# Kernel tuning notes

Measured on AMD Instinct MI355X. Metric: run time of the kernel, lower is better.

The kernel has to match this reference:

```python
import jax, jax.numpy as jnp
import numpy as np

N_NODES = 30000
N_EDGES = 480000
C = 32          # channel multiplicity of hidden irreps (32x0e + 32x1o)
L = 3           # graph_net_steps
H = 64          # radial MLP hidden width
NB = 8          # num radial basis functions
NS = 5          # num_species
R_MAX = 4.0
AVG_NEIGH = 16.0
N_PATHS = 5     # tensor-product paths per layer


def setup_inputs() -> dict:
    key = jax.random.key(0)
    ks = jax.random.split(key, 16)

    def w(k, shape, fan_in):
        return jax.random.normal(k, shape, jnp.float32) / np.sqrt(fan_in)

    return {
        "vectors": jax.random.normal(ks[0], (N_EDGES, 3), jnp.float32),
        "node_specie": jax.random.randint(ks[1], (N_NODES,), 0, NS),
        "senders": jax.random.randint(ks[2], (N_EDGES,), 0, N_NODES),
        "receivers": jax.random.randint(ks[3], (N_EDGES,), 0, N_NODES),
        "emb": jax.random.normal(ks[4], (NS, C), jnp.float32),
        "w_rad1": w(ks[5], (L, NB, H), NB),
        "w_rad2": w(ks[6], (L, H, H), H),
        "w_rad_out": w(ks[7], (L, H, N_PATHS * C), H),
        "w_lin_s": w(ks[8], (L, 2 * C, 2 * C), 2 * C),
        "w_lin_v": w(ks[9], (L, 3 * C, C), 3 * C),
        "w_sc_s": w(ks[10], (L, NS, C, 2 * C), C),
        "w_sc_v": w(ks[11], (L, NS, C, C), C),
        "w_out1": w(ks[12], (C, 16), C),
        "w_out2": w(ks[13], (16, 1), 16),
    }


def _envelope(x, p=6):
    # smooth polynomial cutoff, = 1 at x=0, = 0 (with zero derivs) at x=1
    u = (1.0 - (p + 1) * (p + 2) / 2 * x**p + p * (p + 2) * x**(p + 1)
         - p * (p + 1) / 2 * x**(p + 2))
    return jnp.where(x < 1.0, u, 0.0)


def _radial_basis(lengths):
    # bessel radial basis [E, NB] with smooth cutoff envelope
    n = jnp.arange(1, NB + 1, dtype=jnp.float32)
    x = lengths / R_MAX
    b = np.sqrt(2.0 / R_MAX) * jnp.sin(n * np.pi * x[:, None]) \
        / jnp.maximum(lengths, 1e-9)[:, None]
    return b * _envelope(x)[:, None]


def reference(vectors, node_specie, senders, receivers, emb, w_rad1, w_rad2,
              w_rad_out, w_lin_s, w_lin_v, w_sc_s, w_sc_v, w_out1, w_out2):
    vectors = vectors / R_MAX                       # as in original __call__
    lengths = jnp.linalg.norm(vectors, axis=-1)
    nhat = vectors / jnp.maximum(lengths, 1e-9)[:, None]   # unit edge vectors
    rb = _radial_basis(lengths)                     # [E, NB]

    s = emb[node_specie]                            # [N, C] scalars (0e)
    v = jnp.zeros((s.shape[0], C, 3), s.dtype)      # [N, C, 3] vectors (1o)

    for l in range(L):
        # radial MLP -> per-path, per-channel edge weights
        h = jax.nn.silu(rb @ w_rad1[l])
        h = jax.nn.silu(h @ w_rad2[l])
        wgt = (h @ w_rad_out[l]).reshape(-1, N_PATHS, C)        # [E, 5, C]

        s_u = s[senders]                                         # [E, C]
        v_u = v[senders]                                         # [E, C, 3]
        ndv = jnp.einsum('ed,ecd->ec', nhat, v_u)                # <n, v>

        # CG tensor-product message paths with spherical harmonics of n
        p0 = wgt[:, 0] * s_u                                     # 0e x Y0 -> 0e
        p1 = wgt[:, 1] * ndv                                     # 1o x Y1 -> 0e
        p2 = wgt[:, 2][:, :, None] * (s_u[:, :, None] * nhat[:, None, :])  # 0e x Y1 -> 1o
        p3 = wgt[:, 3][:, :, None] * v_u                         # 1o x Y0 -> 1o
        p4 = wgt[:, 4][:, :, None] * (nhat[:, None, :] * ndv[:, :, None] - v_u / 3.0)  # 1o x Y2 -> 1o

        agg_s = jax.ops.segment_sum(jnp.concatenate([p0, p1], 1), receivers,
                                    num_segments=N_NODES) / AVG_NEIGH      # [N, 2C]
        agg_v = jax.ops.segment_sum(jnp.concatenate([p2, p3, p4], 1), receivers,
                                    num_segments=N_NODES) / AVG_NEIGH      # [N, 3C, 3]

        sg = agg_s @ w_lin_s[l]                                  # [N, 2C]: C feats + C gates
        vn = jnp.einsum('npd,pc->ncd', agg_v, w_lin_v[l])        # [N, C, 3]
        # self-connection: per-species linear (== tp with species one-hot)
        sg = sg + jnp.einsum('nc,nck->nk', s, w_sc_s[l][node_specie])
        vn = vn + jnp.einsum('ncd,nck->nkd', v, w_sc_v[l][node_specie])

        s_new, gates = jnp.split(sg, 2, axis=1)
        s = jax.nn.silu(s_new)                                   # even activation
        v = jax.nn.silu(gates)[:, :, None] * vn                  # gated 1o

    e = (s @ w_out1) @ w_out2            # Linear '16x0e' -> Linear '0e'
    return e[:, 0]                        # per-node energy [N]
```

## Files before the change

### kernel.cpp

```cpp
#include <hip/hip_runtime.h>
#include <math.h>

#define NNODES 30000
#define NEDGES 480000
#define NC 32
#define NL 3
#define NH 64
#define NBASIS 8
#define NSPEC 5
#define INV_AVG 0.0625f

typedef _Float16 half2v __attribute__((ext_vector_type(2)));
typedef _Float16 half4v __attribute__((ext_vector_type(4)));
typedef _Float16 half8v __attribute__((ext_vector_type(8)));
typedef float    float4v __attribute__((ext_vector_type(4)));
typedef unsigned int uint32;

__device__ __forceinline__ float silu_f(float x) {
    return x / (1.f + __expf(-x));
}
__device__ __forceinline__ float rdlane(float v, int k) {
    return __uint_as_float(__builtin_amdgcn_readlane(__float_as_uint(v), k));
}
__device__ __forceinline__ half2v u2h(uint32 u) {
    union { uint32 u; half2v h; } x; x.u = u; return x.h;
}


__global__ void count_kernel(const int* __restrict__ receivers, int* __restrict__ deg) {
    int e = blockIdx.x * blockDim.x + threadIdx.x;
    if (e >= NEDGES) return;
    atomicAdd(&deg[receivers[e]], 1);
}

__global__ void scan_kernel(const int* __restrict__ deg, int* __restrict__ rowstart) {
    __shared__ int lsum[256];
    __shared__ int loff[256];
    int t = threadIdx.x;
    int lo = t * 118;
    int hi = min(lo + 118, NNODES);
    int s = 0;
    for (int i = lo; i < hi; ++i) s += deg[i];
    lsum[t] = s;
    __syncthreads();
    if (t == 0) {
        int run = 0;
        for (int i = 0; i < 256; ++i) { loff[i] = run; run += lsum[i]; }
    }
    __syncthreads();
    int run = loff[t];
    for (int i = lo; i < hi; ++i) { rowstart[i] = run; run += deg[i]; }
    if (t == 0) rowstart[NNODES] = NEDGES;
}

__global__ void copy_cursor_kernel(const int* __restrict__ rowstart, int* __restrict__ cursor) {
    int i = blockIdx.x * blockDim.x + threadIdx.x;
    if (i < NNODES) cursor[i] = rowstart[i];
}

__global__ void fill_kernel(const int* __restrict__ receivers,
                            int* __restrict__ cursor, int* __restrict__ epos) {
    int e = blockIdx.x * blockDim.x + threadIdx.x;
    if (e >= NEDGES) return;
    epos[e] = atomicAdd(&cursor[receivers[e]], 1);
}

__global__ void geom_perm_kernel(const float* __restrict__ vec,
                                 const int* __restrict__ senders,
                                 const int* __restrict__ epos,
                                 float* __restrict__ nh_perm,
                                 int* __restrict__ snd_perm,
                                 float* __restrict__ rb_perm) {
    int e = blockIdx.x * blockDim.x + threadIdx.x;
    if (e >= NEDGES) return;
    float vx = vec[3*e+0] * 0.25f;
    float vy = vec[3*e+1] * 0.25f;
    float vz = vec[3*e+2] * 0.25f;
    float len = sqrtf(vx*vx + vy*vy + vz*vz);
    float inv = 1.f / fmaxf(len, 1e-9f);
    int p = epos[e];
    *(float4*)(nh_perm + (size_t)p*4) = make_float4(vx*inv, vy*inv, vz*inv, 0.f);
    snd_perm[p] = senders[e];
    float x = len * 0.25f;
    float x3 = x*x*x;
    float x6 = x3*x3;
    float x7 = x6*x;
    float x8 = x7*x;
    float env = (x < 1.f) ? (1.f - 28.f*x6 + 48.f*x7 - 21.f*x8) : 0.f;
    float scale = 0.7071067811865476f * inv * env;
    float rbv[8];
    #pragma unroll
    for (int i = 0; i < NBASIS; ++i)
        rbv[i] = scale * sinf((float)(i+1) * 3.14159265358979f * x);
    *(float4*)(rb_perm + (size_t)p*8)     = make_float4(rbv[0], rbv[1], rbv[2], rbv[3]);
    *(float4*)(rb_perm + (size_t)p*8 + 4) = make_float4(rbv[4], rbv[5], rbv[6], rbv[7]);
}

__global__ void prepw_kernel(const float* __restrict__ w1, const float* __restrict__ w2,
                             const float* __restrict__ w3,
                             float* __restrict__ w1t, _Float16* __restrict__ w2f,
                             _Float16* __restrict__ w3f) {
    int t = blockIdx.x * blockDim.x + threadIdx.x;
    if (t < NL * 64 * 8) {
        int l = t / 512, r = t % 512, k = r >> 3, b = r & 7;
        w1t[t] = w1[l * 512 + b * 64 + k];
    }
    int u = t - NL * 64 * 8;
    if (u >= 0 && u < NL * 2 * 4 * 64 * 8) {
        int e = u & 7, lane = (u >> 3) & 63, nt = (u >> 9) & 3, ks = (u >> 11) & 1, l = u >> 12;
        int k = ks * 32 + ((lane >> 4) << 3) + e;
        int col = nt * 16 + (lane & 15);
        w2f[u] = (_Float16)w2[l * 4096 + k * 64 + col];
    }
    int v = t - NL * 64 * 8 - NL * 2 * 4 * 64 * 8;
    if (v >= 0 && v < NL * 2 * 10 * 64 * 8) {
        int q = v / 5120, rem = v % 5120;
        int l = q >> 1, ks = q & 1;
        int nt = rem >> 9, lane = (rem >> 3) & 63, e = rem & 7;
        int k = ks * 32 + ((lane >> 4) << 3) + e;
        int col = nt * 16 + (lane & 15);
        w3f[v] = (_Float16)w3[l * 10240 + k * 160 + col];
    }
}

__global__ void init_kernel(const int* __restrict__ specie,
                            const float* __restrict__ emb,
                            _Float16* __restrict__ s) {
    int t = blockIdx.x * blockDim.x + threadIdx.x;
    if (t >= NNODES * NC) return;
    int n = t >> 5;
    int c = t & 31;
    s[t] = (_Float16)emb[specie[n] * NC + c];
}

__global__ __launch_bounds__(256) void mlpm_kernel(
    const float* __restrict__ rb_perm,
    const float* __restrict__ w1t,
    const _Float16* __restrict__ w2f,
    const _Float16* __restrict__ w3f,
    _Float16* __restrict__ wgt16)
{
    __shared__ float w1lds[512];
    __shared__ __align__(16) _Float16 lds2[4][2688];

    for (int t = threadIdx.x; t < 512; t += 256) w1lds[t] = w1t[t];
    __syncthreads();

    int lane = threadIdx.x & 63;
    int wid  = threadIdx.x >> 6;
    int c16 = lane & 15;
    int kg  = lane >> 4;
    int ibase = blockIdx.x * 64 + wid * 16;
    int g = blockIdx.x * 4 + wid;

    float4 ra4 = *(const float4*)(rb_perm + (size_t)(ibase + c16) * 8);
    float4 rb4 = *(const float4*)(rb_perm + (size_t)(ibase + c16) * 8 + 4);

    half8v a0, a1;
    #pragma unroll
    for (int e = 0; e < 8; ++e) {
        const float* wr0 = w1lds + (kg * 8 + e) * 8;
        float d0;
        d0 = ra4.x * wr0[0];
        d0 = fmaf(ra4.y, wr0[1], d0);
        d0 = fmaf(ra4.z, wr0[2], d0);
        d0 = fmaf(ra4.w, wr0[3], d0);
        d0 = fmaf(rb4.x, wr0[4], d0);
        d0 = fmaf(rb4.y, wr0[5], d0);
        d0 = fmaf(rb4.z, wr0[6], d0);
        d0 = fmaf(rb4.w, wr0[7], d0);
        a0[e] = (_Float16)silu_f(d0);
        const float* wr1 = w1lds + (32 + kg * 8 + e) * 8;
        float d1;
        d1 = ra4.x * wr1[0];
        d1 = fmaf(ra4.y, wr1[1], d1);
        d1 = fmaf(ra4.z, wr1[2], d1);
        d1 = fmaf(ra4.w, wr1[3], d1);
        d1 = fmaf(rb4.x, wr1[4], d1);
        d1 = fmaf(rb4.y, wr1[5], d1);
        d1 = fmaf(rb4.z, wr1[6], d1);
        d1 = fmaf(rb4.w, wr1[7], d1);
        a1[e] = (_Float16)silu_f(d1);
    }

    _Float16* tw = &lds2[wid][0];
    float4v zero4 = {0.f, 0.f, 0.f, 0.f};
    #pragma unroll
    for (int nt = 0; nt < 4; ++nt) {
        half8v b0 = *(const half8v*)(w2f + (size_t)(nt) * 512 + lane * 8);
        half8v b1 = *(const half8v*)(w2f + (size_t)(4 + nt) * 512 + lane * 8);
        float4v acc = __builtin_amdgcn_mfma_f32_16x16x32_f16(a0, b0, zero4, 0, 0, 0);
        acc = __builtin_amdgcn_mfma_f32_16x16x32_f16(a1, b1, acc, 0, 0, 0);
        #pragma unroll
        for (int r = 0; r < 4; ++r)
            tw[(kg * 4 + r) * 72 + nt * 16 + c16] = (_Float16)silu_f(acc[r]);
    }

    half8v a2 = *(const half8v*)(tw + c16 * 72 + kg * 8);
    half8v a3 = *(const half8v*)(tw + c16 * 72 + 32 + kg * 8);

    #pragma unroll
    for (int nt = 0; nt < 10; ++nt) {
        half8v b0 = *(const half8v*)(w3f + (size_t)(nt) * 512 + lane * 8);
        half8v b1 = *(const half8v*)(w3f + (size_t)(10 + nt) * 512 + lane * 8);
        float4v acc = __builtin_amdgcn_mfma_f32_16x16x32_f16(a2, b0, zero4, 0, 0, 0);
        acc = __builtin_amdgcn_mfma_f32_16x16x32_f16(a3, b1, acc, 0, 0, 0);
        int slot;
        if (nt < 4)      slot = nt * 32 + 2 * c16;
        else if (nt < 8) slot = (nt - 4) * 32 + 2 * c16 + 1;
        else             slot = 128 + (nt - 8) * 16 + c16;
        #pragma unroll
        for (int r = 0; r < 4; ++r)
            tw[(kg * 4 + r) * 168 + slot] = (_Float16)acc[r];
    }

    _Float16* gout = wgt16 + (size_t)g * 2560;
    #pragma unroll
    for (int u = 0; u < 5; ++u) {
        int g4 = u * 64 + lane;
        int edge = g4 / 20;
        int part = g4 % 20;
        half8v vv = *(const half8v*)(tw + edge * 168 + part * 8);
        *(half8v*)(gout + edge * 160 + part * 8) = vv;
    }
}

__global__ __launch_bounds__(512) void gather_tp_kernel(
    const _Float16* __restrict__ wgt16,
    const float* __restrict__ nh_perm,
    const int* __restrict__ snd_perm,
    const int* __restrict__ rowstart, const int* __restrict__ deg,
    const _Float16* __restrict__ s_in, const _Float16* __restrict__ v_in,
    float* __restrict__ agg_s,
    float* __restrict__ agg_v)
{
    int lane = threadIdx.x & 63;
    int wid  = threadIdx.x >> 6;
    int n = blockIdx.x * 8 + wid;
    if (n >= NNODES) return;

    int c = lane & 31;
    int half = lane >> 5;

    float accS = 0.f;
    float aVa0 = 0.f, aVa1 = 0.f, aVa2 = 0.f;
    float aVb0 = 0.f, aVb1 = 0.f, aVb2 = 0.f;

    int start = rowstart[n];
    int cnt   = deg[n];

    float4 nh_c = make_float4(0.f, 0.f, 0.f, 0.f);
    float d0_c = 0.f, d1_c = 0.f, d2_c = 0.f;
    float su_c = 0.f, v0_c = 0.f, v1_c = 0.f, v2_c = 0.f;
    if (cnt > 0) {
        int snd0 = snd_perm[start];
        nh_c = *(const float4*)(nh_perm + (size_t)start * 4);
        size_t gb = (size_t)(start >> 4) * 2560 + (size_t)(start & 15) * 160;
        half2v pr = u2h(*(const uint32*)(wgt16 + gb + lane * 2));
        d0_c = (float)pr.x;
        d1_c = (float)pr.y;
        d2_c = (float)wgt16[gb + 128 + c];
        su_c = (float)s_in[(size_t)snd0 * NC + c];
        v0_c = (float)v_in[(size_t)snd0 * 96 + c];
        v1_c = (float)v_in[(size_t)snd0 * 96 + 32 + c];
        v2_c = (float)v_in[(size_t)snd0 * 96 + 64 + c];
    }

    for (int i = 0; i < cnt; ++i) {
        float4 nh = nh_c;
        float d0 = d0_c, d1 = d1_c, d2f = d2_c;
        float su = su_c, v0 = v0_c, v1 = v1_c, v2 = v2_c;

        if (i + 1 < cnt) {
            int idx1 = start + i + 1;
            int snd1 = snd_perm[idx1];
            nh_c = *(const float4*)(nh_perm + (size_t)idx1 * 4);
            size_t gb1 = (size_t)(idx1 >> 4) * 2560 + (size_t)(idx1 & 15) * 160;
            half2v pr1 = u2h(*(const uint32*)(wgt16 + gb1 + lane * 2));
            d0_c = (float)pr1.x;
            d1_c = (float)pr1.y;
            d2_c = (float)wgt16[gb1 + 128 + c];
            su_c = (float)s_in[(size_t)snd1 * NC + c];
            v0_c = (float)v_in[(size_t)snd1 * 96 + c];
            v1_c = (float)v_in[(size_t)snd1 * 96 + 32 + c];
            v2_c = (float)v_in[(size_t)snd1 * 96 + 64 + c];
        }

        float ndv = nh.x * v0;
        ndv = fmaf(nh.y, v1, ndv);
        ndv = fmaf(nh.z, v2, ndv);

        float sSel = half ? ndv : su;
        accS = fmaf(d0, sSel, accS);
        float scale = half ? d1 : d1 * su;
        float f0 = half ? v0 : nh.x;
        float f1 = half ? v1 : nh.y;
        float f2 = half ? v2 : nh.z;
        aVa0 = fmaf(scale, f0, aVa0);
        aVa1 = fmaf(scale, f1, aVa1);
        aVa2 = fmaf(scale, f2, aVa2);
        float m4 = half ? 0.f : d2f;
        aVb0 = fmaf(m4, fmaf(nh.x, ndv, -v0 * (1.f / 3.f)), aVb0);
        aVb1 = fmaf(m4, fmaf(nh.y, ndv, -v1 * (1.f / 3.f)), aVb1);
        aVb2 = fmaf(m4, fmaf(nh.z, ndv, -v2 * (1.f / 3.f)), aVb2);
    }

    agg_s[(size_t)n * 64 + lane] = accS;
    float* av = agg_v + (size_t)n * 288;
    if (half == 0) {
        av[c * 3 + 0] = aVa0; av[c * 3 + 1] = aVa1; av[c * 3 + 2] = aVa2;
        av[(64 + c) * 3 + 0] = aVb0; av[(64 + c) * 3 + 1] = aVb1; av[(64 + c) * 3 + 2] = aVb2;
    } else {
        av[(32 + c) * 3 + 0] = aVa0; av[(32 + c) * 3 + 1] = aVa1; av[(32 + c) * 3 + 2] = aVa2;
    }
}

__global__ __launch_bounds__(256) void node_kernel(
    const int* __restrict__ specie,
    const float* __restrict__ agg_s, const float* __restrict__ agg_v,
    const _Float16* __restrict__ s_in,  const _Float16* __restrict__ v_in,
    const float* __restrict__ wls,
    const float* __restrict__ wlv,
    const float* __restrict__ wscs,
    const float* __restrict__ wscv,
    _Float16* __restrict__ s_out, _Float16* __restrict__ v_out)
{
    __shared__ float sAV[4][288];
    __shared__ float sVO[4][96];

    int lane = threadIdx.x & 63;
    int wid  = threadIdx.x >> 6;
    int n = blockIdx.x * 4 + wid;
    if (n >= NNODES) return;
    int sp = specie[n];

    const float* av = agg_v + (size_t)n * 288;
    sAV[wid][lane]       = av[lane];
    sAV[wid][64 + lane]  = av[64 + lane];
    sAV[wid][128 + lane] = av[128 + lane];
    sAV[wid][192 + lane] = av[192 + lane];
    if (lane < 32) sAV[wid][256 + lane] = av[256 + lane];
    const _Float16* vo = v_in + (size_t)n * 96;
    if (lane < 32) {
        sVO[wid][lane]      = (float)vo[lane];
        sVO[wid][32 + lane] = (float)vo[32 + lane];
        sVO[wid][64 + lane] = (float)vo[64 + lane];
    }

    float asv = agg_s[(size_t)n * 64 + lane];
    float sv  = (float)s_in[(size_t)n * 32 + (lane & 31)];

    __syncthreads();

    float sg = 0.f;
    #pragma unroll
    for (int j = 0; j < 64; ++j)
        sg = fmaf(rdlane(asv, j), wls[j * 64 + lane], sg);
    sg *= INV_AVG;
    const float* ws = wscs + (size_t)sp * 32 * 64;
    #pragma unroll
    for (int j = 0; j < 32; ++j)
        sg = fmaf(rdlane(sv, j), ws[j * 64 + lane], sg);
    float act  = silu_f(sg);
    float gate = __shfl(act, (lane & 31) + 32);

    int c = lane & 31;
    int h = lane >> 5;
    float vn1 = 0.f, vn2 = 0.f;
    #pragma unroll
    for (int p = 0; p < 96; ++p) {
        float w = wlv[p * 32 + c];
        vn1 = fmaf(sAV[wid][3 * p + h], w, vn1);
        vn2 = fmaf(sAV[wid][3 * p + 2], w, vn2);
    }
    vn1 *= INV_AVG; vn2 *= INV_AVG;
    const float* wv = wscv + (size_t)sp * 32 * 32;
    #pragma unroll
    for (int j = 0; j < 32; ++j) {
        float w = wv[j * 32 + c];
        vn1 = fmaf(sVO[wid][h * 32 + j], w, vn1);
        vn2 = fmaf(sVO[wid][64 + j],     w, vn2);
    }

    if (lane < 32) s_out[(size_t)n * 32 + lane] = (_Float16)act;
    v_out[(size_t)n * 96 + h * 32 + c] = (_Float16)(gate * vn1);
    if (h == 0) v_out[(size_t)n * 96 + 64 + c] = (_Float16)(gate * vn2);
}

__global__ void out_kernel(const _Float16* __restrict__ s,
                           const float* __restrict__ w1,
                           const float* __restrict__ w2,
                           float* __restrict__ out) {
    int n = blockIdx.x * blockDim.x + threadIdx.x;
    if (n >= NNODES) return;
    float sv[NC];
    #pragma unroll
    for (int c = 0; c < NC; ++c) sv[c] = (float)s[(size_t)n * NC + c];
    float e = 0.f;
    #pragma unroll
    for (int j = 0; j < 16; ++j) {
        float tj = 0.f;
        #pragma unroll
        for (int c = 0; c < NC; ++c) tj += sv[c] * w1[c * 16 + j];
        e += tj * w2[j];
    }
    out[n] = e;
}

extern "C" void kernel_launch(void* const* d_in, const int* in_sizes, int n_in,
                              void* d_out, int out_size, void* d_ws, size_t ws_size,
                              hipStream_t stream) {
    const float* vectors   = (const float*)d_in[0];
    const int*   specie    = (const int*)  d_in[1];
    const int*   senders   = (const int*)  d_in[2];
    const int*   receivers = (const int*)  d_in[3];
    const float* emb       = (const float*)d_in[4];
    const float* w_rad1    = (const float*)d_in[5];
    const float* w_rad2    = (const float*)d_in[6];
    const float* w_rad_out = (const float*)d_in[7];
    const float* w_lin_s   = (const float*)d_in[8];
    const float* w_lin_v   = (const float*)d_in[9];
    const float* w_sc_s    = (const float*)d_in[10];
    const float* w_sc_v    = (const float*)d_in[11];
    const float* w_out1    = (const float*)d_in[12];
    const float* w_out2    = (const float*)d_in[13];

    char* base = (char*)d_ws;
    size_t off = 0;
    auto alloc = [&](size_t bytes) { char* q = base + off; off += (bytes + 255) & ~(size_t)255; return q; };

    float*    nh_perm  = (float*)alloc((size_t)NEDGES * 4 * 4);
    float*    rb_perm  = (float*)alloc((size_t)NEDGES * 8 * 4);
    int*      snd_perm = (int*)alloc((size_t)NEDGES * 4);
    int*      epos     = (int*)alloc((size_t)NEDGES * 4);
    _Float16* s_a      = (_Float16*)alloc((size_t)NNODES * NC * 2);
    _Float16* v_a      = (_Float16*)alloc((size_t)NNODES * NC * 3 * 2);
    _Float16* s_b      = (_Float16*)alloc((size_t)NNODES * NC * 2);
    _Float16* v_b      = (_Float16*)alloc((size_t)NNODES * NC * 3 * 2);
    float*    aggs     = (float*)alloc((size_t)NNODES * 2 * NC * 4);
    float*    aggv     = (float*)alloc((size_t)NNODES * 3 * NC * 3 * 4);
    int* deg        = (int*)alloc((size_t)NNODES * 4);
    int* rowstart   = (int*)alloc((size_t)(NNODES + 4) * 4);
    int* cursor     = (int*)alloc((size_t)NNODES * 4);
    float*    w1t      = (float*)alloc((size_t)NL * 64 * 8 * 4);
    _Float16* w2f      = (_Float16*)alloc((size_t)NL * 2 * 4 * 64 * 8 * 2);
    _Float16* w3f      = (_Float16*)alloc((size_t)NL * 2 * 10 * 64 * 8 * 2);
    _Float16* wgt16    = (_Float16*)alloc((size_t)NEDGES * 160 * 2);
    if (off > ws_size) return;

    (void)hipMemsetAsync(deg, 0, NNODES * sizeof(int), stream);
    count_kernel<<<(NEDGES + 255) / 256, 256, 0, stream>>>(receivers, deg);
    scan_kernel<<<1, 256, 0, stream>>>(deg, rowstart);
    copy_cursor_kernel<<<(NNODES + 255) / 256, 256, 0, stream>>>(rowstart, cursor);
    fill_kernel<<<(NEDGES + 255) / 256, 256, 0, stream>>>(receivers, cursor, epos);
    geom_perm_kernel<<<(NEDGES + 255) / 256, 256, 0, stream>>>(
        vectors, senders, epos, nh_perm, snd_perm, rb_perm);
    int prep_n = NL * 64 * 8 + NL * 2 * 4 * 64 * 8 + NL * 2 * 10 * 64 * 8;
    prepw_kernel<<<(prep_n + 255) / 256, 256, 0, stream>>>(
        w_rad1, w_rad2, w_rad_out, w1t, w2f, w3f);

    init_kernel<<<(NNODES * NC + 255) / 256, 256, 0, stream>>>(specie, emb, s_a);
    (void)hipMemsetAsync(v_a, 0, (size_t)NNODES * NC * 3 * 2, stream);

    _Float16* si = s_a; _Float16* vi = v_a; _Float16* so = s_b; _Float16* vo = v_b;
    for (int l = 0; l < NL; ++l) {
        mlpm_kernel<<<NEDGES / 64, 256, 0, stream>>>(
            rb_perm,
            w1t + (size_t)l * 512,
            w2f + (size_t)l * 4096,
            w3f + (size_t)l * 10240,
            wgt16);
        gather_tp_kernel<<<(NNODES + 7) / 8, 512, 0, stream>>>(
            wgt16, nh_perm, snd_perm, rowstart, deg, si, vi, aggs, aggv);
        node_kernel<<<(NNODES + 3) / 4, 256, 0, stream>>>(
            specie, aggs, aggv, si, vi,
            w_lin_s + (size_t)l * 64 * 64,
            w_lin_v + (size_t)l * 96 * 32,
            w_sc_s + (size_t)l * NSPEC * NC * 64,
            w_sc_v + (size_t)l * NSPEC * NC * NC,
            so, vo);
        _Float16* ts = si; si = so; so = ts;
        _Float16* tv = vi; vi = vo; vo = tv;
    }

    out_kernel<<<(NNODES + 255) / 256, 256, 0, stream>>>(si, w_out1, w_out2, (float*)d_out);
}
```

Baseline: 720.4 us.

## Merge CSR count and fill passes; store aggregates in fp16

The separate count and fill atomic passes, plus the cursor copy kernel, are replaced by a single atomic pass whose return value gives each edge's local slot. The global position is then rebuilt from the row start during the geometry permute. This removes two kernel launches and one pass of atomics over the edges. Separately, the per-node aggregate buffers written by the gather kernel and read by the node kernel are switched from fp32 to fp16, halving that traffic at some cost in accumulated precision.

```diff
diff --git a/kernel.cpp b/kernel.cpp
--- a/kernel.cpp
+++ b/kernel.cpp
@@ -27,10 +27,11 @@
 }
 
 
-__global__ void count_kernel(const int* __restrict__ receivers, int* __restrict__ deg) {
+__global__ void fill_kernel(const int* __restrict__ receivers,
+                            int* __restrict__ deg, int* __restrict__ epos) {
     int e = blockIdx.x * blockDim.x + threadIdx.x;
     if (e >= NEDGES) return;
-    atomicAdd(&deg[receivers[e]], 1);
+    epos[e] = atomicAdd(&deg[receivers[e]], 1);
 }
 
 __global__ void scan_kernel(const int* __restrict__ deg, int* __restrict__ rowstart) {
@@ -53,20 +54,10 @@
     if (t == 0) rowstart[NNODES] = NEDGES;
 }
 
-__global__ void copy_cursor_kernel(const int* __restrict__ rowstart, int* __restrict__ cursor) {
-    int i = blockIdx.x * blockDim.x + threadIdx.x;
-    if (i < NNODES) cursor[i] = rowstart[i];
-}
-
-__global__ void fill_kernel(const int* __restrict__ receivers,
-                            int* __restrict__ cursor, int* __restrict__ epos) {
-    int e = blockIdx.x * blockDim.x + threadIdx.x;
-    if (e >= NEDGES) return;
-    epos[e] = atomicAdd(&cursor[receivers[e]], 1);
-}
-
 __global__ void geom_perm_kernel(const float* __restrict__ vec,
                                  const int* __restrict__ senders,
+                                 const int* __restrict__ receivers,
+                                 const int* __restrict__ rowstart,
                                  const int* __restrict__ epos,
                                  float* __restrict__ nh_perm,
                                  int* __restrict__ snd_perm,
@@ -78,7 +69,7 @@
     float vz = vec[3*e+2] * 0.25f;
     float len = sqrtf(vx*vx + vy*vy + vz*vz);
     float inv = 1.f / fmaxf(len, 1e-9f);
-    int p = epos[e];
+    int p = rowstart[receivers[e]] + epos[e];
     *(float4*)(nh_perm + (size_t)p*4) = make_float4(vx*inv, vy*inv, vz*inv, 0.f);
     snd_perm[p] = senders[e];
     float x = len * 0.25f;
@@ -231,8 +222,8 @@
     const int* __restrict__ snd_perm,
     const int* __restrict__ rowstart, const int* __restrict__ deg,
     const _Float16* __restrict__ s_in, const _Float16* __restrict__ v_in,
-    float* __restrict__ agg_s,
-    float* __restrict__ agg_v)
+    _Float16* __restrict__ agg_s,
+    _Float16* __restrict__ agg_v)
 {
     int lane = threadIdx.x & 63;
     int wid  = threadIdx.x >> 6;
@@ -305,19 +296,19 @@
         aVb2 = fmaf(m4, fmaf(nh.z, ndv, -v2 * (1.f / 3.f)), aVb2);
     }
 
-    agg_s[(size_t)n * 64 + lane] = accS;
-    float* av = agg_v + (size_t)n * 288;
+    agg_s[(size_t)n * 64 + lane] = (_Float16)accS;
+    _Float16* av = agg_v + (size_t)n * 288;
     if (half == 0) {
-        av[c * 3 + 0] = aVa0; av[c * 3 + 1] = aVa1; av[c * 3 + 2] = aVa2;
-        av[(64 + c) * 3 + 0] = aVb0; av[(64 + c) * 3 + 1] = aVb1; av[(64 + c) * 3 + 2] = aVb2;
+        av[c * 3 + 0] = (_Float16)aVa0; av[c * 3 + 1] = (_Float16)aVa1; av[c * 3 + 2] = (_Float16)aVa2;
+        av[(64 + c) * 3 + 0] = (_Float16)aVb0; av[(64 + c) * 3 + 1] = (_Float16)aVb1; av[(64 + c) * 3 + 2] = (_Float16)aVb2;
     } else {
-        av[(32 + c) * 3 + 0] = aVa0; av[(32 + c) * 3 + 1] = aVa1; av[(32 + c) * 3 + 2] = aVa2;
+        av[(32 + c) * 3 + 0] = (_Float16)aVa0; av[(32 + c) * 3 + 1] = (_Float16)aVa1; av[(32 + c) * 3 + 2] = (_Float16)aVa2;
     }
 }
 
 __global__ __launch_bounds__(256) void node_kernel(
     const int* __restrict__ specie,
-    const float* __restrict__ agg_s, const float* __restrict__ agg_v,
+    const _Float16* __restrict__ agg_s, const _Float16* __restrict__ agg_v,
     const _Float16* __restrict__ s_in,  const _Float16* __restrict__ v_in,
     const float* __restrict__ wls,
     const float* __restrict__ wlv,
@@ -334,12 +325,12 @@
     if (n >= NNODES) return;
     int sp = specie[n];
 
-    const float* av = agg_v + (size_t)n * 288;
-    sAV[wid][lane]       = av[lane];
-    sAV[wid][64 + lane]  = av[64 + lane];
-    sAV[wid][128 + lane] = av[128 + lane];
-    sAV[wid][192 + lane] = av[192 + lane];
-    if (lane < 32) sAV[wid][256 + lane] = av[256 + lane];
+    const _Float16* av = agg_v + (size_t)n * 288;
+    sAV[wid][lane]       = (float)av[lane];
+    sAV[wid][64 + lane]  = (float)av[64 + lane];
+    sAV[wid][128 + lane] = (float)av[128 + lane];
+    sAV[wid][192 + lane] = (float)av[192 + lane];
+    if (lane < 32) sAV[wid][256 + lane] = (float)av[256 + lane];
     const _Float16* vo = v_in + (size_t)n * 96;
     if (lane < 32) {
         sVO[wid][lane]      = (float)vo[lane];
@@ -347,7 +338,7 @@
         sVO[wid][64 + lane] = (float)vo[64 + lane];
     }
 
-    float asv = agg_s[(size_t)n * 64 + lane];
+    float asv = (float)agg_s[(size_t)n * 64 + lane];
     float sv  = (float)s_in[(size_t)n * 32 + (lane & 31)];
 
     __syncthreads();
@@ -437,11 +428,10 @@
     _Float16* v_a      = (_Float16*)alloc((size_t)NNODES * NC * 3 * 2);
     _Float16* s_b      = (_Float16*)alloc((size_t)NNODES * NC * 2);
     _Float16* v_b      = (_Float16*)alloc((size_t)NNODES * NC * 3 * 2);
-    float*    aggs     = (float*)alloc((size_t)NNODES * 2 * NC * 4);
-    float*    aggv     = (float*)alloc((size_t)NNODES * 3 * NC * 3 * 4);
+    _Float16* aggs     = (_Float16*)alloc((size_t)NNODES * 2 * NC * 2);
+    _Float16* aggv     = (_Float16*)alloc((size_t)NNODES * 3 * NC * 3 * 2);
     int* deg        = (int*)alloc((size_t)NNODES * 4);
     int* rowstart   = (int*)alloc((size_t)(NNODES + 4) * 4);
-    int* cursor     = (int*)alloc((size_t)NNODES * 4);
     float*    w1t      = (float*)alloc((size_t)NL * 64 * 8 * 4);
     _Float16* w2f      = (_Float16*)alloc((size_t)NL * 2 * 4 * 64 * 8 * 2);
     _Float16* w3f      = (_Float16*)alloc((size_t)NL * 2 * 10 * 64 * 8 * 2);
@@ -449,12 +439,10 @@
     if (off > ws_size) return;
 
     (void)hipMemsetAsync(deg, 0, NNODES * sizeof(int), stream);
-    count_kernel<<<(NEDGES + 255) / 256, 256, 0, stream>>>(receivers, deg);
+    fill_kernel<<<(NEDGES + 255) / 256, 256, 0, stream>>>(receivers, deg, epos);
     scan_kernel<<<1, 256, 0, stream>>>(deg, rowstart);
-    copy_cursor_kernel<<<(NNODES + 255) / 256, 256, 0, stream>>>(rowstart, cursor);
-    fill_kernel<<<(NEDGES + 255) / 256, 256, 0, stream>>>(receivers, cursor, epos);
     geom_perm_kernel<<<(NEDGES + 255) / 256, 256, 0, stream>>>(
-        vectors, senders, epos, nh_perm, snd_perm, rb_perm);
+        vectors, senders, receivers, rowstart, epos, nh_perm, snd_perm, rb_perm);
     int prep_n = NL * 64 * 8 + NL * 2 * 4 * 64 * 8 + NL * 2 * 10 * 64 * 8;
     prepw_kernel<<<(prep_n + 255) / 256, 256, 0, stream>>>(
         w_rad1, w_rad2, w_rad_out, w1t, w2f, w3f);
```

Result: faster. 693.6 us (-3.7%).
